# Kernel tuning notes

Hardware: AMD Instinct MI355X
Metric: run time of the kernel (lower is better)

The kernel has to match this reference:

```python
import jax, jax.numpy as jnp
import numpy as np

B, N, D, H = 1, 2048, 2048, 16
K = D // H  # head dim = 128


def setup_inputs() -> dict:
    key = jax.random.key(0)
    k1, k2, k3 = jax.random.split(key, 3)
    x = jax.random.normal(k1, (B, N, D), dtype=jnp.float32)
    # torch Linear(D, 3D, bias=False): y = x @ W.T; we store the transposed weight directly.
    W_qkv = jax.random.normal(k2, (D, 3 * D), dtype=jnp.float32) * 0.02
    W_out = jax.random.normal(k3, (D, D), dtype=jnp.float32) * 0.02
    return {"x": x, "W_qkv": W_qkv, "W_out": W_out}


def reference(x, W_qkv, W_out):
    b, n, d = x.shape
    qkv = (x @ W_qkv).reshape(b, n, 3, H, K)  # [B,N,3,H,K]
    q, k, v = qkv[:, :, 0], qkv[:, :, 1], qkv[:, :, 2]  # each [B,N,H,K]
    scale = np.float32(1.0 / np.sqrt(K))
    scores = jnp.einsum('bnhk,bmhk->bnhm', q, k) * scale  # [B,N,H,M]
    causal_mask = jnp.tril(jnp.ones((n, n), dtype=bool))  # [N,M]
    scores = jnp.where(causal_mask[None, :, None, :], scores, jnp.float32(-jnp.inf))
    probs = jax.nn.softmax(scores, axis=-1)
    attn = jnp.einsum('bnhm,bmhk->bnhk', probs, v).reshape(b, n, d)
    return attn @ W_out
```

## Files before the change

kernel.cpp:

```cpp
#include <hip/hip_runtime.h>
#include <hip/hip_bf16.h>
#include <math.h>

#define N_SEQ  2048
#define DMODEL 2048
#define NHEAD  16
#define HDIM   128
#define QKV_LD 6144

typedef __attribute__((ext_vector_type(8))) short bf16x8;
typedef __attribute__((ext_vector_type(4))) float f32x4;

__device__ __forceinline__ ushort f2bf(float x) {
    union { float f; unsigned u; } v; v.f = x;
    unsigned r = (v.u + 0x7fffu + ((v.u >> 16) & 1u)) >> 16;
    return (ushort)r;
}
__device__ __forceinline__ float bf2f(ushort h) {
    union { unsigned u; float f; } v; v.u = ((unsigned)h) << 16;
    return v.f;
}

__global__ __launch_bounds__(256)
void convert_split(const float* __restrict__ in, ushort* __restrict__ oh,
                   ushort* __restrict__ ol, int n4)
{
    int i = blockIdx.x * 256 + threadIdx.x;
    if (i >= n4) return;
    float4 v = ((const float4*)in)[i];
    ushort4 h, l;
    h.x = f2bf(v.x); l.x = f2bf(v.x - bf2f(h.x));
    h.y = f2bf(v.y); l.y = f2bf(v.y - bf2f(h.y));
    h.z = f2bf(v.z); l.z = f2bf(v.z - bf2f(h.z));
    h.w = f2bf(v.w); l.w = f2bf(v.w - bf2f(h.w));
    ((ushort4*)oh)[i] = h;
    ((ushort4*)ol)[i] = l;
}

__global__ __launch_bounds__(256)
void convert_split_t(const float* __restrict__ in, ushort* __restrict__ oh,
                     ushort* __restrict__ ol, int R, int C)
{
    __shared__ float T[64][65];
    const int t = threadIdx.x;
    const int c0 = blockIdx.x * 64, r0 = blockIdx.y * 64;
    #pragma unroll
    for (int p = 0; p < 4; ++p) {
        int r = (t >> 4) + p * 16;
        int c4 = (t & 15) * 4;
        float4 v = *(const float4*)&in[(size_t)(r0 + r) * C + c0 + c4];
        T[r][c4] = v.x; T[r][c4 + 1] = v.y; T[r][c4 + 2] = v.z; T[r][c4 + 3] = v.w;
    }
    __syncthreads();
    #pragma unroll
    for (int p = 0; p < 4; ++p) {
        int c = (t >> 4) + p * 16;
        int r4 = (t & 15) * 4;
        float f0 = T[r4][c], f1 = T[r4 + 1][c], f2 = T[r4 + 2][c], f3 = T[r4 + 3][c];
        ushort4 h, l;
        h.x = f2bf(f0); l.x = f2bf(f0 - bf2f(h.x));
        h.y = f2bf(f1); l.y = f2bf(f1 - bf2f(h.y));
        h.z = f2bf(f2); l.z = f2bf(f2 - bf2f(h.z));
        h.w = f2bf(f3); l.w = f2bf(f3 - bf2f(h.w));
        *(ushort4*)&oh[(size_t)(c0 + c) * R + r0 + r4] = h;
        *(ushort4*)&ol[(size_t)(c0 + c) * R + r0 + r4] = l;
    }
}

__global__ __launch_bounds__(256)
void transpose_v(const ushort* __restrict__ qkvh, ushort* __restrict__ vt)
{
    __shared__ ushort T[64][72];
    const int t = threadIdx.x;
    const int c0 = blockIdx.x * 64, n0 = blockIdx.y * 64;
    #pragma unroll
    for (int p = 0; p < 2; ++p) {
        int r = (t >> 3) + p * 32;
        int u = (t & 7) * 8;
        *(bf16x8*)&T[r][u] = *(const bf16x8*)&qkvh[(size_t)(n0 + r) * QKV_LD + 2 * DMODEL + c0 + u];
    }
    __syncthreads();
    #pragma unroll
    for (int p = 0; p < 2; ++p) {
        int d = (t >> 3) + p * 32;
        int ju = (t & 7) * 8;
        bf16x8 o;
        #pragma unroll
        for (int i = 0; i < 8; ++i) o[i] = (short)T[ju + i][d];
        *(bf16x8*)&vt[(size_t)(c0 + d) * N_SEQ + n0 + ju] = o;
    }
}

template<bool BF16OUT>
__global__ __launch_bounds__(256, 2)
void gemm_bf16x3(const ushort* __restrict__ Ah_g, const ushort* __restrict__ Al_g,
                 const ushort* __restrict__ Bh_g, const ushort* __restrict__ Bl_g,
                 ushort* __restrict__ Ch, ushort* __restrict__ Cl,
                 float* __restrict__ Cf, int M, int N, int K)
{
    __shared__ ushort Ah[128 * 40], Al[128 * 40], Bh[128 * 40], Bl[128 * 40];
    const int t = threadIdx.x;
    const int l = t & 63;
    const int w = t >> 6;
    const int l15 = l & 15, kgr = l >> 4;
    const int wm = (w >> 1) * 64, wn = (w & 1) * 64;
    const int bm = blockIdx.y * 128, bn = blockIdx.x * 128;
    const int sr = t >> 2, sku = (t & 3) * 8;

    f32x4 acc[4][4] = {};
    bf16x8 sA[4], sB[4];

    auto load_stage = [&](int k0) {
        const size_t a0 = (size_t)(bm + sr) * K + k0 + sku;
        const size_t a1 = (size_t)(bm + sr + 64) * K + k0 + sku;
        sA[0] = *(const bf16x8*)(Ah_g + a0);
        sA[1] = *(const bf16x8*)(Ah_g + a1);
        sA[2] = *(const bf16x8*)(Al_g + a0);
        sA[3] = *(const bf16x8*)(Al_g + a1);
        const size_t b0 = (size_t)(bn + sr) * K + k0 + sku;
        const size_t b1 = (size_t)(bn + sr + 64) * K + k0 + sku;
        sB[0] = *(const bf16x8*)(Bh_g + b0);
        sB[1] = *(const bf16x8*)(Bh_g + b1);
        sB[2] = *(const bf16x8*)(Bl_g + b0);
        sB[3] = *(const bf16x8*)(Bl_g + b1);
    };
    auto write_stage = [&]() {
        *(bf16x8*)&Ah[sr * 40 + sku]        = sA[0];
        *(bf16x8*)&Ah[(sr + 64) * 40 + sku] = sA[1];
        *(bf16x8*)&Al[sr * 40 + sku]        = sA[2];
        *(bf16x8*)&Al[(sr + 64) * 40 + sku] = sA[3];
        *(bf16x8*)&Bh[sr * 40 + sku]        = sB[0];
        *(bf16x8*)&Bh[(sr + 64) * 40 + sku] = sB[1];
        *(bf16x8*)&Bl[sr * 40 + sku]        = sB[2];
        *(bf16x8*)&Bl[(sr + 64) * 40 + sku] = sB[3];
    };

    load_stage(0);
    for (int k0 = 0; k0 < K; k0 += 32) {
        __syncthreads();
        write_stage();
        __syncthreads();
        if (k0 + 32 < K) load_stage(k0 + 32);

        bf16x8 ah[4], al[4], bh[4], bl[4];
        #pragma unroll
        for (int mf = 0; mf < 4; ++mf) {
            ah[mf] = *(const bf16x8*)&Ah[(wm + mf * 16 + l15) * 40 + kgr * 8];
            al[mf] = *(const bf16x8*)&Al[(wm + mf * 16 + l15) * 40 + kgr * 8];
        }
        #pragma unroll
        for (int nf = 0; nf < 4; ++nf) {
            bh[nf] = *(const bf16x8*)&Bh[(wn + nf * 16 + l15) * 40 + kgr * 8];
            bl[nf] = *(const bf16x8*)&Bl[(wn + nf * 16 + l15) * 40 + kgr * 8];
        }
        #pragma unroll
        for (int mf = 0; mf < 4; ++mf)
            #pragma unroll
            for (int nf = 0; nf < 4; ++nf) {
                acc[mf][nf] = __builtin_amdgcn_mfma_f32_16x16x32_bf16(ah[mf], bh[nf], acc[mf][nf], 0, 0, 0);
                acc[mf][nf] = __builtin_amdgcn_mfma_f32_16x16x32_bf16(ah[mf], bl[nf], acc[mf][nf], 0, 0, 0);
                acc[mf][nf] = __builtin_amdgcn_mfma_f32_16x16x32_bf16(al[mf], bh[nf], acc[mf][nf], 0, 0, 0);
            }
    }

    #pragma unroll
    for (int mf = 0; mf < 4; ++mf)
        #pragma unroll
        for (int nf = 0; nf < 4; ++nf)
            #pragma unroll
            for (int r = 0; r < 4; ++r) {
                const int m = bm + wm + mf * 16 + kgr * 4 + r;
                const int n = bn + wn + nf * 16 + l15;
                const float v = acc[mf][nf][r];
                if constexpr (BF16OUT) {
                    ushort h = f2bf(v);
                    Ch[(size_t)m * N + n] = h;
                    Cl[(size_t)m * N + n] = f2bf(v - bf2f(h));
                } else {
                    Cf[(size_t)m * N + n] = v;
                }
            }
}

__global__ __launch_bounds__(256, 2)
void attn_mfma(const ushort* __restrict__ qkvh, const ushort* __restrict__ qkvl,
               const ushort* __restrict__ vt,
               ushort* __restrict__ oh, ushort* __restrict__ ol)
{
    __shared__ ushort Kh[64 * 136], Kl[64 * 136], Vts[128 * 72], St[4 * 16 * 72];
    const int t = threadIdx.x;
    const int l = t & 63;
    const int w = t >> 6;
    const int l15 = l & 15, kgr = l >> 4;
    const int h = blockIdx.y, qb = blockIdx.x;
    const int q0 = qb * 64 + w * 16;

    bf16x8 qh[4], ql[4];
    {
        const size_t base = (size_t)(q0 + l15) * QKV_LD + h * HDIM;
        #pragma unroll
        for (int kc = 0; kc < 4; ++kc) {
            qh[kc] = *(const bf16x8*)(qkvh + base + kc * 32 + kgr * 8);
            ql[kc] = *(const bf16x8*)(qkvl + base + kc * 32 + kgr * 8);
        }
    }

    f32x4 o[8] = {};
    float m_run[4], l_run[4];
    #pragma unroll
    for (int r = 0; r < 4; ++r) { m_run[r] = -1e30f; l_run[r] = 0.f; }

    bf16x8 sKh[4], sKl[4], sV[4];
    auto load_tile = [&](int jb) {
        #pragma unroll
        for (int i = 0; i < 4; ++i) {
            int r = (t >> 4) + i * 16;
            size_t g = (size_t)(jb + r) * QKV_LD + DMODEL + h * HDIM + (t & 15) * 8;
            sKh[i] = *(const bf16x8*)(qkvh + g);
            sKl[i] = *(const bf16x8*)(qkvl + g);
        }
        #pragma unroll
        for (int i = 0; i < 4; ++i) {
            int d = (t >> 3) + i * 32;
            sV[i] = *(const bf16x8*)(vt + (size_t)(h * HDIM + d) * N_SEQ + jb + (t & 7) * 8);
        }
    };
    auto write_tile = [&]() {
        #pragma unroll
        for (int i = 0; i < 4; ++i) {
            int r = (t >> 4) + i * 16;
            *(bf16x8*)&Kh[r * 136 + (t & 15) * 8] = sKh[i];
            *(bf16x8*)&Kl[r * 136 + (t & 15) * 8] = sKl[i];
        }
        #pragma unroll
        for (int i = 0; i < 4; ++i) {
            int d = (t >> 3) + i * 32;
            *(bf16x8*)&Vts[d * 72 + (t & 7) * 8] = sV[i];
        }
    };

    const float scale = 0.08838834764831845f;

    load_tile(0);
    for (int jt = 0; jt <= qb; ++jt) {
        const int jb = jt * 64;
        __syncthreads();
        write_tile();
        __syncthreads();
        if (jt < qb) load_tile(jb + 64);

        float sv[4][4];
        #pragma unroll
        for (int jf = 0; jf < 4; ++jf) {
            f32x4 sacc = {};
            #pragma unroll
            for (int kc = 0; kc < 4; ++kc) {
                bf16x8 kh = *(const bf16x8*)&Kh[(jf * 16 + l15) * 136 + kc * 32 + kgr * 8];
                bf16x8 kl = *(const bf16x8*)&Kl[(jf * 16 + l15) * 136 + kc * 32 + kgr * 8];
                sacc = __builtin_amdgcn_mfma_f32_16x16x32_bf16(qh[kc], kh, sacc, 0, 0, 0);
                sacc = __builtin_amdgcn_mfma_f32_16x16x32_bf16(qh[kc], kl, sacc, 0, 0, 0);
                sacc = __builtin_amdgcn_mfma_f32_16x16x32_bf16(ql[kc], kh, sacc, 0, 0, 0);
            }
            const int j = jb + jf * 16 + l15;
            #pragma unroll
            for (int r = 0; r < 4; ++r) {
                const int q = q0 + kgr * 4 + r;
                sv[jf][r] = (j > q) ? -1e30f : sacc[r] * scale;
            }
        }

        float corr[4], p[4][4];
        #pragma unroll
        for (int r = 0; r < 4; ++r) {
            float tm = fmaxf(fmaxf(sv[0][r], sv[1][r]), fmaxf(sv[2][r], sv[3][r]));
            tm = fmaxf(tm, __shfl_xor(tm, 1));
            tm = fmaxf(tm, __shfl_xor(tm, 2));
            tm = fmaxf(tm, __shfl_xor(tm, 4));
            tm = fmaxf(tm, __shfl_xor(tm, 8));
            const float nm = fmaxf(m_run[r], tm);
            corr[r] = __expf(m_run[r] - nm);
            m_run[r] = nm;
            float rs = 0.f;
            #pragma unroll
            for (int jf = 0; jf < 4; ++jf) { p[jf][r] = __expf(sv[jf][r] - nm); rs += p[jf][r]; }
            rs += __shfl_xor(rs, 1);
            rs += __shfl_xor(rs, 2);
            rs += __shfl_xor(rs, 4);
            rs += __shfl_xor(rs, 8);
            l_run[r] = l_run[r] * corr[r] + rs;
        }

        #pragma unroll
        for (int jf = 0; jf < 4; ++jf)
            #pragma unroll
            for (int r = 0; r < 4; ++r)
                St[w * 1152 + (kgr * 4 + r) * 72 + jf * 16 + l15] = f2bf(p[jf][r]);

        #pragma unroll
        for (int df = 0; df < 8; ++df)
            #pragma unroll
            for (int r = 0; r < 4; ++r) o[df][r] *= corr[r];

        #pragma unroll
        for (int jc = 0; jc < 2; ++jc) {
            bf16x8 pa = *(const bf16x8*)&St[w * 1152 + l15 * 72 + jc * 32 + kgr * 8];
            #pragma unroll
            for (int df = 0; df < 8; ++df) {
                bf16x8 vb = *(const bf16x8*)&Vts[(df * 16 + l15) * 72 + jc * 32 + kgr * 8];
                o[df] = __builtin_amdgcn_mfma_f32_16x16x32_bf16(pa, vb, o[df], 0, 0, 0);
            }
        }
    }

    #pragma unroll
    for (int r = 0; r < 4; ++r) l_run[r] = 1.f / l_run[r];
    #pragma unroll
    for (int df = 0; df < 8; ++df)
        #pragma unroll
        for (int r = 0; r < 4; ++r) {
            const float v = o[df][r] * l_run[r];
            const size_t a = (size_t)(q0 + kgr * 4 + r) * DMODEL + h * HDIM + df * 16 + l15;
            const ushort hh = f2bf(v);
            oh[a] = hh;
            ol[a] = f2bf(v - bf2f(hh));
        }
}

#define BM 128
#define BN 128
#define BKG 16

__global__ __launch_bounds__(256, 2)
void gemm_f32(const float* __restrict__ A, const float* __restrict__ B,
              float* __restrict__ C, int M, int N, int K,
              int lda, int ldb, int ldc)
{
    __shared__ float As[BKG][132];
    __shared__ float Bs[BKG][132];
    const int t = threadIdx.x;
    const int tx = t & 15, ty = t >> 4;
    const int bm = blockIdx.y * BM, bn = blockIdx.x * BN;
    const int am = t >> 2, ak = (t & 3) << 2;
    const int bk = t >> 5, bn4 = (t & 31) << 2;
    float acc[8][8];
    #pragma unroll
    for (int i = 0; i < 8; ++i)
        #pragma unroll
        for (int j = 0; j < 8; ++j) acc[i][j] = 0.f;
    for (int k0 = 0; k0 < K; k0 += BKG) {
        const float4 a0 = *(const float4*)&A[(size_t)(bm + am) * lda + k0 + ak];
        const float4 a1 = *(const float4*)&A[(size_t)(bm + am + 64) * lda + k0 + ak];
        const float4 b0 = *(const float4*)&B[(size_t)(k0 + bk) * ldb + bn + bn4];
        const float4 b1 = *(const float4*)&B[(size_t)(k0 + bk + 8) * ldb + bn + bn4];
        __syncthreads();
        As[ak + 0][am] = a0.x; As[ak + 1][am] = a0.y; As[ak + 2][am] = a0.z; As[ak + 3][am] = a0.w;
        As[ak + 0][am + 64] = a1.x; As[ak + 1][am + 64] = a1.y; As[ak + 2][am + 64] = a1.z; As[ak + 3][am + 64] = a1.w;
        *(float4*)&Bs[bk][bn4] = b0;
        *(float4*)&Bs[bk + 8][bn4] = b1;
        __syncthreads();
        #pragma unroll
        for (int kk = 0; kk < BKG; ++kk) {
            const float4 A0 = *(const float4*)&As[kk][ty << 2];
            const float4 A1 = *(const float4*)&As[kk][(ty << 2) + 64];
            const float4 B0 = *(const float4*)&Bs[kk][tx << 2];
            const float4 B1 = *(const float4*)&Bs[kk][(tx << 2) + 64];
            const float a[8] = {A0.x, A0.y, A0.z, A0.w, A1.x, A1.y, A1.z, A1.w};
            const float b[8] = {B0.x, B0.y, B0.z, B0.w, B1.x, B1.y, B1.z, B1.w};
            #pragma unroll
            for (int i = 0; i < 8; ++i)
                #pragma unroll
                for (int j = 0; j < 8; ++j) acc[i][j] = fmaf(a[i], b[j], acc[i][j]);
        }
    }
    #pragma unroll
    for (int i = 0; i < 8; ++i) {
        const int m = bm + ((i < 4) ? ((ty << 2) + i) : (64 + (ty << 2) + i - 4));
        const float4 o0 = make_float4(acc[i][0], acc[i][1], acc[i][2], acc[i][3]);
        const float4 o1 = make_float4(acc[i][4], acc[i][5], acc[i][6], acc[i][7]);
        *(float4*)&C[(size_t)m * ldc + bn + (tx << 2)] = o0;
        *(float4*)&C[(size_t)m * ldc + bn + 64 + (tx << 2)] = o1;
    }
}

#define QB 64
#define KB 64
#define PQT 68

__device__ __forceinline__ int swz(int c, int k) { return c ^ ((k >> 3) & 7); }

__global__ __launch_bounds__(256, 1)
void attn_f32(const float* __restrict__ qkv, float* __restrict__ out)
{
    __shared__ float Qt[HDIM][PQT];
    __shared__ float Kt[HDIM][PQT];
    __shared__ float Vs[KB][132];
    __shared__ float Sf[KB][PQT];
    __shared__ float pmax[4][QB];
    __shared__ float psum[4][QB];
    __shared__ float rowm[QB];
    __shared__ float rowstat[QB];
    const int t = threadIdx.x;
    const int h = blockIdx.y, qb = blockIdx.x;
    const int row0 = qb * QB;
    const int lc = t & 31, lr = t >> 5;
    {
        const float* qbase = qkv + (size_t)row0 * QKV_LD + h * HDIM;
        #pragma unroll
        for (int r = 0; r < 8; ++r) {
            const int m = lr + r * 8;
            const float4 q = *(const float4*)&qbase[(size_t)m * QKV_LD + (lc << 2)];
            const int kb4 = lc << 2;
            Qt[kb4 + 0][(swz(m >> 2, kb4 + 0) << 2) + (m & 3)] = q.x;
            Qt[kb4 + 1][(swz(m >> 2, kb4 + 1) << 2) + (m & 3)] = q.y;
            Qt[kb4 + 2][(swz(m >> 2, kb4 + 2) << 2) + (m & 3)] = q.z;
            Qt[kb4 + 3][(swz(m >> 2, kb4 + 3) << 2) + (m & 3)] = q.w;
        }
    }
    float m_run = -3.0e38f, l_run = 0.f;
    float o[4][8];
    #pragma unroll
    for (int i = 0; i < 4; ++i)
        #pragma unroll
        for (int j = 0; j < 8; ++j) o[i][j] = 0.f;
    const int cq = t & 15, cj = t >> 4;
    const int om = (t >> 4) << 2, oc = (t & 15) << 2;
    const int srow = t & 63, sseg = t >> 6;
    const float scale = 0.08838834764831845f;
    const int ntiles = qb + 1;
    for (int jt = 0; jt < ntiles; ++jt) {
        const int jbase = jt * KB;
        float4 kreg[8], vreg[8];
        {
            const float* kbaseg = qkv + (size_t)jbase * QKV_LD + DMODEL + h * HDIM;
            const float* vbaseg = qkv + (size_t)jbase * QKV_LD + 2 * DMODEL + h * HDIM;
            #pragma unroll
            for (int r = 0; r < 8; ++r) {
                const int j = lr + r * 8;
                kreg[r] = *(const float4*)&kbaseg[(size_t)j * QKV_LD + (lc << 2)];
                vreg[r] = *(const float4*)&vbaseg[(size_t)j * QKV_LD + (lc << 2)];
            }
        }
        __syncthreads();
        {
            const int kb4 = lc << 2;
            #pragma unroll
            for (int r = 0; r < 8; ++r) {
                const int j = lr + r * 8;
                Kt[kb4 + 0][(swz(j >> 2, kb4 + 0) << 2) + (j & 3)] = kreg[r].x;
                Kt[kb4 + 1][(swz(j >> 2, kb4 + 1) << 2) + (j & 3)] = kreg[r].y;
                Kt[kb4 + 2][(swz(j >> 2, kb4 + 2) << 2) + (j & 3)] = kreg[r].z;
                Kt[kb4 + 3][(swz(j >> 2, kb4 + 3) << 2) + (j & 3)] = kreg[r].w;
                *(float4*)&Vs[j][kb4] = vreg[r];
            }
        }
        __syncthreads();
        float s[4][4];
        #pragma unroll
        for (int i = 0; i < 4; ++i)
            #pragma unroll
            for (int j = 0; j < 4; ++j) s[i][j] = 0.f;
        #pragma unroll 8
        for (int k = 0; k < HDIM; ++k) {
            const float4 qv = *(const float4*)&Qt[k][swz(cq, k) << 2];
            const float4 kv = *(const float4*)&Kt[k][swz(cj, k) << 2];
            const float qa[4] = {qv.x, qv.y, qv.z, qv.w};
            const float ka[4] = {kv.x, kv.y, kv.z, kv.w};
            #pragma unroll
            for (int mm = 0; mm < 4; ++mm)
                #pragma unroll
                for (int jj = 0; jj < 4; ++jj) s[mm][jj] = fmaf(qa[mm], ka[jj], s[mm][jj]);
        }
        const bool diag = (jt == qb);
        #pragma unroll
        for (int jj = 0; jj < 4; ++jj)
            #pragma unroll
            for (int mm = 0; mm < 4; ++mm) {
                float v = s[mm][jj] * scale;
                if (diag && (jbase + (cj << 2) + jj > row0 + (cq << 2) + mm)) v = -1.0e30f;
                Sf[(cj << 2) + jj][(cq << 2) + mm] = v;
            }
        __syncthreads();
        {
            float tmax = -3.0e38f;
            #pragma unroll
            for (int i = 0; i < 16; ++i) tmax = fmaxf(tmax, Sf[(sseg << 4) + i][srow]);
            pmax[sseg][srow] = tmax;
        }
        __syncthreads();
        if (t < QB) {
            float nm = fmaxf(fmaxf(pmax[0][t], pmax[1][t]), fmaxf(pmax[2][t], pmax[3][t]));
            nm = fmaxf(m_run, nm);
            rowm[t] = nm;
            rowstat[t] = __expf(m_run - nm);
            m_run = nm;
        }
        __syncthreads();
        {
            const float nm = rowm[srow];
            float rsum = 0.f;
            #pragma unroll
            for (int i = 0; i < 16; ++i) {
                const int j = (sseg << 4) + i;
                const float p = __expf(Sf[j][srow] - nm);
                Sf[j][srow] = p;
                rsum += p;
            }
            psum[sseg][srow] = rsum;
        }
        __syncthreads();
        if (t < QB) {
            l_run = l_run * rowstat[t] + (psum[0][t] + psum[1][t] + psum[2][t] + psum[3][t]);
        }
        {
            const float c0 = rowstat[om + 0], c1 = rowstat[om + 1];
            const float c2 = rowstat[om + 2], c3 = rowstat[om + 3];
            #pragma unroll
            for (int c = 0; c < 8; ++c) { o[0][c] *= c0; o[1][c] *= c1; o[2][c] *= c2; o[3][c] *= c3; }
            #pragma unroll 4
            for (int j = 0; j < KB; ++j) {
                const float4 p = *(const float4*)&Sf[j][om];
                const float4 v0 = *(const float4*)&Vs[j][oc];
                const float4 v1 = *(const float4*)&Vs[j][oc + 64];
                const float pa[4] = {p.x, p.y, p.z, p.w};
                const float va[8] = {v0.x, v0.y, v0.z, v0.w, v1.x, v1.y, v1.z, v1.w};
                #pragma unroll
                for (int mm = 0; mm < 4; ++mm)
                    #pragma unroll
                    for (int c = 0; c < 8; ++c) o[mm][c] = fmaf(pa[mm], va[c], o[mm][c]);
            }
        }
    }
    __syncthreads();
    if (t < QB) rowstat[t] = 1.f / l_run;
    __syncthreads();
    float* obase = out + (size_t)row0 * DMODEL + h * HDIM;
    #pragma unroll
    for (int mm = 0; mm < 4; ++mm) {
        const float inv = rowstat[om + mm];
        const float4 r0 = make_float4(o[mm][0] * inv, o[mm][1] * inv, o[mm][2] * inv, o[mm][3] * inv);
        const float4 r1 = make_float4(o[mm][4] * inv, o[mm][5] * inv, o[mm][6] * inv, o[mm][7] * inv);
        *(float4*)&obase[(size_t)(om + mm) * DMODEL + oc] = r0;
        *(float4*)&obase[(size_t)(om + mm) * DMODEL + 64 + oc] = r1;
    }
}

extern "C" void kernel_launch(void* const* d_in, const int* in_sizes, int n_in,
                              void* d_out, int out_size, void* d_ws, size_t ws_size,
                              hipStream_t stream)
{
    const float* x    = (const float*)d_in[0];
    const float* Wqkv = (const float*)d_in[1];
    const float* Wout = (const float*)d_in[2];
    float* outp = (float*)d_out;

    const size_t O_XHI = 0;
    const size_t O_XLO = 8388608;
    const size_t O_WT  = 16777216;
    const size_t O_QKV = 67108864;
    const size_t NEED  = 117440512;

    char* ws = (char*)d_ws;
    if (ws_size >= NEED) {
        ushort* x_hi   = (ushort*)(ws + O_XHI);
        ushort* x_lo   = (ushort*)(ws + O_XLO);
        ushort* wqt_hi = (ushort*)(ws + O_WT);
        ushort* wqt_lo = (ushort*)(ws + O_WT + 25165824);
        ushort* qkv_hi = (ushort*)(ws + O_QKV);
        ushort* qkv_lo = (ushort*)(ws + O_QKV + 25165824);
        ushort* wot_hi = (ushort*)(ws + O_WT);
        ushort* wot_lo = (ushort*)(ws + O_WT + 8388608);
        ushort* vt     = (ushort*)(ws + O_WT + 16777216);
        ushort* at_hi  = (ushort*)(ws + O_XHI);
        ushort* at_lo  = (ushort*)(ws + O_XLO);

        convert_split<<<dim3(N_SEQ * DMODEL / 4 / 256), 256, 0, stream>>>(
            x, x_hi, x_lo, N_SEQ * DMODEL / 4);
        convert_split_t<<<dim3(QKV_LD / 64, DMODEL / 64), 256, 0, stream>>>(
            Wqkv, wqt_hi, wqt_lo, DMODEL, QKV_LD);
        gemm_bf16x3<true><<<dim3(QKV_LD / 128, N_SEQ / 128), 256, 0, stream>>>(
            x_hi, x_lo, wqt_hi, wqt_lo, qkv_hi, qkv_lo, nullptr,
            N_SEQ, QKV_LD, DMODEL);
        convert_split_t<<<dim3(DMODEL / 64, DMODEL / 64), 256, 0, stream>>>(
            Wout, wot_hi, wot_lo, DMODEL, DMODEL);
        transpose_v<<<dim3(DMODEL / 64, N_SEQ / 64), 256, 0, stream>>>(qkv_hi, vt);
        attn_mfma<<<dim3(N_SEQ / 64, NHEAD), 256, 0, stream>>>(
            qkv_hi, qkv_lo, vt, at_hi, at_lo);
        gemm_bf16x3<false><<<dim3(DMODEL / 128, N_SEQ / 128), 256, 0, stream>>>(
            at_hi, at_lo, wot_hi, wot_lo, nullptr, nullptr, outp,
            N_SEQ, DMODEL, DMODEL);
    } else {
        float* qkv  = (float*)d_ws;
        float* attn = qkv + (size_t)N_SEQ * QKV_LD;
        gemm_f32<<<dim3(QKV_LD / BN, N_SEQ / BM), 256, 0, stream>>>(
            x, Wqkv, qkv, N_SEQ, QKV_LD, DMODEL, DMODEL, QKV_LD, QKV_LD);
        attn_f32<<<dim3(N_SEQ / QB, NHEAD), 256, 0, stream>>>(qkv, attn);
        gemm_f32<<<dim3(DMODEL / BN, N_SEQ / BM), 256, 0, stream>>>(
            attn, Wout, outp, N_SEQ, DMODEL, DMODEL, DMODEL, DMODEL, DMODEL);
    }
}
```

Before: 474.2 us.

## Add 256x256-tile double-buffered bf16x3 GEMM for QKV projection

Replaces the QKV projection GEMM with a new kernel using 256x256 tiles, 512 threads, double-buffered LDS with register prefetch, and an XCD-grouped block index remap. Hi/lo split data are interleaved per row in LDS. The goal is more data reuse per tile and loads that overlap compute. The trade-off is a large LDS footprint and only 192 workgroups, fewer than the CU count. The fp32 fallback path is also removed.

```diff
diff --git a/kernel.cpp b/kernel.cpp
--- a/kernel.cpp
+++ b/kernel.cpp
@@ -89,6 +89,109 @@
         for (int i = 0; i < 8; ++i) o[i] = (short)T[ju + i][d];
         *(bf16x8*)&vt[(size_t)(c0 + d) * N_SEQ + n0 + ju] = o;
     }
+}
+
+#define GBM 256
+#define GBN 256
+#define GBK 32
+#define GPITCH 68
+
+template<bool BF16OUT>
+__global__ __launch_bounds__(512, 2)
+void gemm_bf16x3_v2(const ushort* __restrict__ Ah_g, const ushort* __restrict__ Al_g,
+                    const ushort* __restrict__ Bh_g, const ushort* __restrict__ Bl_g,
+                    ushort* __restrict__ Ch, ushort* __restrict__ Cl,
+                    float* __restrict__ Cf, int M, int N, int K)
+{
+    __shared__ ushort bufA[2][GBM * GPITCH];
+    __shared__ ushort bufB[2][GBN * GPITCH];
+
+    const int t = threadIdx.x;
+    const int l = t & 63;
+    const int w = t >> 6;
+    const int l15 = l & 15, kgr = l >> 4;
+    const int wm = (w >> 2) * 128;
+    const int wn = (w & 3) * 64;
+
+    const int nbx = N / GBN, nby = M / GBM;
+    const int nwg = nbx * nby;
+    int flat = blockIdx.x + blockIdx.y * nbx;
+    if ((nwg & 7) == 0) flat = (flat & 7) * (nwg >> 3) + (flat >> 3);
+    const int bm = (flat / nbx) * GBM;
+    const int bn = (flat % nbx) * GBN;
+
+    const int rA = t >> 1;
+    const int hA = t & 1;
+    const ushort* gA = (hA ? Al_g : Ah_g) + (size_t)(bm + rA) * K;
+    const ushort* gB = (hA ? Bl_g : Bh_g) + (size_t)(bn + rA) * K;
+
+    bf16x8 stA[4], stB[4];
+    auto load_regs = [&](int k0) {
+        #pragma unroll
+        for (int j = 0; j < 4; ++j) {
+            stA[j] = *(const bf16x8*)(gA + k0 + j * 8);
+            stB[j] = *(const bf16x8*)(gB + k0 + j * 8);
+        }
+    };
+    auto write_lds = [&](int b) {
+        #pragma unroll
+        for (int j = 0; j < 4; ++j) {
+            *(bf16x8*)&bufA[b][rA * GPITCH + hA * 32 + j * 8] = stA[j];
+            *(bf16x8*)&bufB[b][rA * GPITCH + hA * 32 + j * 8] = stB[j];
+        }
+    };
+
+    f32x4 acc[8][4] = {};
+
+    const int nt = K / GBK;
+    load_regs(0);
+    write_lds(0);
+    load_regs(GBK);
+
+    for (int i = 0; i < nt; ++i) {
+        const int c = i & 1;
+        asm volatile("s_waitcnt lgkmcnt(0)\n\ts_barrier" ::: "memory");
+        if (i + 1 < nt) write_lds(c ^ 1);
+        if (i + 2 < nt) load_regs((i + 2) * GBK);
+
+        bf16x8 bh[4], bl[4];
+        #pragma unroll
+        for (int nf = 0; nf < 4; ++nf) {
+            const int r = wn + nf * 16 + l15;
+            bh[nf] = *(const bf16x8*)&bufB[c][r * GPITCH + kgr * 8];
+            bl[nf] = *(const bf16x8*)&bufB[c][r * GPITCH + 32 + kgr * 8];
+        }
+        #pragma unroll
+        for (int mf = 0; mf < 8; ++mf) {
+            const int r = wm + mf * 16 + l15;
+            bf16x8 ah = *(const bf16x8*)&bufA[c][r * GPITCH + kgr * 8];
+            bf16x8 al = *(const bf16x8*)&bufA[c][r * GPITCH + 32 + kgr * 8];
+            #pragma unroll
+            for (int nf = 0; nf < 4; ++nf) {
+                acc[mf][nf] = __builtin_amdgcn_mfma_f32_16x16x32_bf16(ah, bh[nf], acc[mf][nf], 0, 0, 0);
+                acc[mf][nf] = __builtin_amdgcn_mfma_f32_16x16x32_bf16(ah, bl[nf], acc[mf][nf], 0, 0, 0);
+                acc[mf][nf] = __builtin_amdgcn_mfma_f32_16x16x32_bf16(al, bh[nf], acc[mf][nf], 0, 0, 0);
+            }
+        }
+    }
+
+    #pragma unroll
+    for (int mf = 0; mf < 8; ++mf)
+        #pragma unroll
+        for (int nf = 0; nf < 4; ++nf)
+            #pragma unroll
+            for (int r = 0; r < 4; ++r) {
+                const int m = bm + wm + mf * 16 + kgr * 4 + r;
+                const int n = bn + wn + nf * 16 + l15;
+                const float v = acc[mf][nf][r];
+                if constexpr (BF16OUT) {
+                    ushort h = f2bf(v);
+                    Ch[(size_t)m * N + n] = h;
+                    Cl[(size_t)m * N + n] = f2bf(v - bf2f(h));
+                } else {
+                    Cf[(size_t)m * N + n] = v;
+                }
+            }
 }
 
 template<bool BF16OUT>
@@ -326,224 +429,6 @@
         }
 }
 
-#define BM 128
-#define BN 128
-#define BKG 16
-
-__global__ __launch_bounds__(256, 2)
-void gemm_f32(const float* __restrict__ A, const float* __restrict__ B,
-              float* __restrict__ C, int M, int N, int K,
-              int lda, int ldb, int ldc)
-{
-    __shared__ float As[BKG][132];
-    __shared__ float Bs[BKG][132];
-    const int t = threadIdx.x;
-    const int tx = t & 15, ty = t >> 4;
-    const int bm = blockIdx.y * BM, bn = blockIdx.x * BN;
-    const int am = t >> 2, ak = (t & 3) << 2;
-    const int bk = t >> 5, bn4 = (t & 31) << 2;
-    float acc[8][8];
-    #pragma unroll
-    for (int i = 0; i < 8; ++i)
-        #pragma unroll
-        for (int j = 0; j < 8; ++j) acc[i][j] = 0.f;
-    for (int k0 = 0; k0 < K; k0 += BKG) {
-        const float4 a0 = *(const float4*)&A[(size_t)(bm + am) * lda + k0 + ak];
-        const float4 a1 = *(const float4*)&A[(size_t)(bm + am + 64) * lda + k0 + ak];
-        const float4 b0 = *(const float4*)&B[(size_t)(k0 + bk) * ldb + bn + bn4];
-        const float4 b1 = *(const float4*)&B[(size_t)(k0 + bk + 8) * ldb + bn + bn4];
-        __syncthreads();
-        As[ak + 0][am] = a0.x; As[ak + 1][am] = a0.y; As[ak + 2][am] = a0.z; As[ak + 3][am] = a0.w;
-        As[ak + 0][am + 64] = a1.x; As[ak + 1][am + 64] = a1.y; As[ak + 2][am + 64] = a1.z; As[ak + 3][am + 64] = a1.w;
-        *(float4*)&Bs[bk][bn4] = b0;
-        *(float4*)&Bs[bk + 8][bn4] = b1;
-        __syncthreads();
-        #pragma unroll
-        for (int kk = 0; kk < BKG; ++kk) {
-            const float4 A0 = *(const float4*)&As[kk][ty << 2];
-            const float4 A1 = *(const float4*)&As[kk][(ty << 2) + 64];
-            const float4 B0 = *(const float4*)&Bs[kk][tx << 2];
-            const float4 B1 = *(const float4*)&Bs[kk][(tx << 2) + 64];
-            const float a[8] = {A0.x, A0.y, A0.z, A0.w, A1.x, A1.y, A1.z, A1.w};
-            const float b[8] = {B0.x, B0.y, B0.z, B0.w, B1.x, B1.y, B1.z, B1.w};
-            #pragma unroll
-            for (int i = 0; i < 8; ++i)
-                #pragma unroll
-                for (int j = 0; j < 8; ++j) acc[i][j] = fmaf(a[i], b[j], acc[i][j]);
-        }
-    }
-    #pragma unroll
-    for (int i = 0; i < 8; ++i) {
-        const int m = bm + ((i < 4) ? ((ty << 2) + i) : (64 + (ty << 2) + i - 4));
-        const float4 o0 = make_float4(acc[i][0], acc[i][1], acc[i][2], acc[i][3]);
-        const float4 o1 = make_float4(acc[i][4], acc[i][5], acc[i][6], acc[i][7]);
-        *(float4*)&C[(size_t)m * ldc + bn + (tx << 2)] = o0;
-        *(float4*)&C[(size_t)m * ldc + bn + 64 + (tx << 2)] = o1;
-    }
-}
-
-#define QB 64
-#define KB 64
-#define PQT 68
-
-__device__ __forceinline__ int swz(int c, int k) { return c ^ ((k >> 3) & 7); }
-
-__global__ __launch_bounds__(256, 1)
-void attn_f32(const float* __restrict__ qkv, float* __restrict__ out)
-{
-    __shared__ float Qt[HDIM][PQT];
-    __shared__ float Kt[HDIM][PQT];
-    __shared__ float Vs[KB][132];
-    __shared__ float Sf[KB][PQT];
-    __shared__ float pmax[4][QB];
-    __shared__ float psum[4][QB];
-    __shared__ float rowm[QB];
-    __shared__ float rowstat[QB];
-    const int t = threadIdx.x;
-    const int h = blockIdx.y, qb = blockIdx.x;
-    const int row0 = qb * QB;
-    const int lc = t & 31, lr = t >> 5;
-    {
-        const float* qbase = qkv + (size_t)row0 * QKV_LD + h * HDIM;
-        #pragma unroll
-        for (int r = 0; r < 8; ++r) {
-            const int m = lr + r * 8;
-            const float4 q = *(const float4*)&qbase[(size_t)m * QKV_LD + (lc << 2)];
-            const int kb4 = lc << 2;
-            Qt[kb4 + 0][(swz(m >> 2, kb4 + 0) << 2) + (m & 3)] = q.x;
-            Qt[kb4 + 1][(swz(m >> 2, kb4 + 1) << 2) + (m & 3)] = q.y;
-            Qt[kb4 + 2][(swz(m >> 2, kb4 + 2) << 2) + (m & 3)] = q.z;
-            Qt[kb4 + 3][(swz(m >> 2, kb4 + 3) << 2) + (m & 3)] = q.w;
-        }
-    }
-    float m_run = -3.0e38f, l_run = 0.f;
-    float o[4][8];
-    #pragma unroll
-    for (int i = 0; i < 4; ++i)
-        #pragma unroll
-        for (int j = 0; j < 8; ++j) o[i][j] = 0.f;
-    const int cq = t & 15, cj = t >> 4;
-    const int om = (t >> 4) << 2, oc = (t & 15) << 2;
-    const int srow = t & 63, sseg = t >> 6;
-    const float scale = 0.08838834764831845f;
-    const int ntiles = qb + 1;
-    for (int jt = 0; jt < ntiles; ++jt) {
-        const int jbase = jt * KB;
-        float4 kreg[8], vreg[8];
-        {
-            const float* kbaseg = qkv + (size_t)jbase * QKV_LD + DMODEL + h * HDIM;
-            const float* vbaseg = qkv + (size_t)jbase * QKV_LD + 2 * DMODEL + h * HDIM;
-            #pragma unroll
-            for (int r = 0; r < 8; ++r) {
-                const int j = lr + r * 8;
-                kreg[r] = *(const float4*)&kbaseg[(size_t)j * QKV_LD + (lc << 2)];
-                vreg[r] = *(const float4*)&vbaseg[(size_t)j * QKV_LD + (lc << 2)];
-            }
-        }
-        __syncthreads();
-        {
-            const int kb4 = lc << 2;
-            #pragma unroll
-            for (int r = 0; r < 8; ++r) {
-                const int j = lr + r * 8;
-                Kt[kb4 + 0][(swz(j >> 2, kb4 + 0) << 2) + (j & 3)] = kreg[r].x;
-                Kt[kb4 + 1][(swz(j >> 2, kb4 + 1) << 2) + (j & 3)] = kreg[r].y;
-                Kt[kb4 + 2][(swz(j >> 2, kb4 + 2) << 2) + (j & 3)] = kreg[r].z;
-                Kt[kb4 + 3][(swz(j >> 2, kb4 + 3) << 2) + (j & 3)] = kreg[r].w;
-                *(float4*)&Vs[j][kb4] = vreg[r];
-            }
-        }
-        __syncthreads();
-        float s[4][4];
-        #pragma unroll
-        for (int i = 0; i < 4; ++i)
-            #pragma unroll
-            for (int j = 0; j < 4; ++j) s[i][j] = 0.f;
-        #pragma unroll 8
-        for (int k = 0; k < HDIM; ++k) {
-            const float4 qv = *(const float4*)&Qt[k][swz(cq, k) << 2];
-            const float4 kv = *(const float4*)&Kt[k][swz(cj, k) << 2];
-            const float qa[4] = {qv.x, qv.y, qv.z, qv.w};
-            const float ka[4] = {kv.x, kv.y, kv.z, kv.w};
-            #pragma unroll
-            for (int mm = 0; mm < 4; ++mm)
-                #pragma unroll
-                for (int jj = 0; jj < 4; ++jj) s[mm][jj] = fmaf(qa[mm], ka[jj], s[mm][jj]);
-        }
-        const bool diag = (jt == qb);
-        #pragma unroll
-        for (int jj = 0; jj < 4; ++jj)
-            #pragma unroll
-            for (int mm = 0; mm < 4; ++mm) {
-                float v = s[mm][jj] * scale;
-                if (diag && (jbase + (cj << 2) + jj > row0 + (cq << 2) + mm)) v = -1.0e30f;
-                Sf[(cj << 2) + jj][(cq << 2) + mm] = v;
-            }
-        __syncthreads();
-        {
-            float tmax = -3.0e38f;
-            #pragma unroll
-            for (int i = 0; i < 16; ++i) tmax = fmaxf(tmax, Sf[(sseg << 4) + i][srow]);
-            pmax[sseg][srow] = tmax;
-        }
-        __syncthreads();
-        if (t < QB) {
-            float nm = fmaxf(fmaxf(pmax[0][t], pmax[1][t]), fmaxf(pmax[2][t], pmax[3][t]));
-            nm = fmaxf(m_run, nm);
-            rowm[t] = nm;
-            rowstat[t] = __expf(m_run - nm);
-            m_run = nm;
-        }
-        __syncthreads();
-        {
-            const float nm = rowm[srow];
-            float rsum = 0.f;
-            #pragma unroll
-            for (int i = 0; i < 16; ++i) {
-                const int j = (sseg << 4) + i;
-                const float p = __expf(Sf[j][srow] - nm);
-                Sf[j][srow] = p;
-                rsum += p;
-            }
-            psum[sseg][srow] = rsum;
-        }
-        __syncthreads();
-        if (t < QB) {
-            l_run = l_run * rowstat[t] + (psum[0][t] + psum[1][t] + psum[2][t] + psum[3][t]);
-        }
-        {
-            const float c0 = rowstat[om + 0], c1 = rowstat[om + 1];
-            const float c2 = rowstat[om + 2], c3 = rowstat[om + 3];
-            #pragma unroll
-            for (int c = 0; c < 8; ++c) { o[0][c] *= c0; o[1][c] *= c1; o[2][c] *= c2; o[3][c] *= c3; }
-            #pragma unroll 4
-            for (int j = 0; j < KB; ++j) {
-                const float4 p = *(const float4*)&Sf[j][om];
-                const float4 v0 = *(const float4*)&Vs[j][oc];
-                const float4 v1 = *(const float4*)&Vs[j][oc + 64];
-                const float pa[4] = {p.x, p.y, p.z, p.w};
-                const float va[8] = {v0.x, v0.y, v0.z, v0.w, v1.x, v1.y, v1.z, v1.w};
-                #pragma unroll
-                for (int mm = 0; mm < 4; ++mm)
-                    #pragma unroll
-                    for (int c = 0; c < 8; ++c) o[mm][c] = fmaf(pa[mm], va[c], o[mm][c]);
-            }
-        }
-    }
-    __syncthreads();
-    if (t < QB) rowstat[t] = 1.f / l_run;
-    __syncthreads();
-    float* obase = out + (size_t)row0 * DMODEL + h * HDIM;
-    #pragma unroll
-    for (int mm = 0; mm < 4; ++mm) {
-        const float inv = rowstat[om + mm];
-        const float4 r0 = make_float4(o[mm][0] * inv, o[mm][1] * inv, o[mm][2] * inv, o[mm][3] * inv);
-        const float4 r1 = make_float4(o[mm][4] * inv, o[mm][5] * inv, o[mm][6] * inv, o[mm][7] * inv);
-        *(float4*)&obase[(size_t)(om + mm) * DMODEL + oc] = r0;
-        *(float4*)&obase[(size_t)(om + mm) * DMODEL + 64 + oc] = r1;
-    }
-}
-
 extern "C" void kernel_launch(void* const* d_in, const int* in_sizes, int n_in,
                               void* d_out, int out_size, void* d_ws, size_t ws_size,
                               hipStream_t stream)
@@ -557,44 +442,33 @@
     const size_t O_XLO = 8388608;
     const size_t O_WT  = 16777216;
     const size_t O_QKV = 67108864;
-    const size_t NEED  = 117440512;
 
     char* ws = (char*)d_ws;
-    if (ws_size >= NEED) {
-        ushort* x_hi   = (ushort*)(ws + O_XHI);
-        ushort* x_lo   = (ushort*)(ws + O_XLO);
-        ushort* wqt_hi = (ushort*)(ws + O_WT);
-        ushort* wqt_lo = (ushort*)(ws + O_WT + 25165824);
-        ushort* qkv_hi = (ushort*)(ws + O_QKV);
-        ushort* qkv_lo = (ushort*)(ws + O_QKV + 25165824);
-        ushort* wot_hi = (ushort*)(ws + O_WT);
-        ushort* wot_lo = (ushort*)(ws + O_WT + 8388608);
-        ushort* vt     = (ushort*)(ws + O_WT + 16777216);
-        ushort* at_hi  = (ushort*)(ws + O_XHI);
-        ushort* at_lo  = (ushort*)(ws + O_XLO);
-
-        convert_split<<<dim3(N_SEQ * DMODEL / 4 / 256), 256, 0, stream>>>(
-            x, x_hi, x_lo, N_SEQ * DMODEL / 4);
-        convert_split_t<<<dim3(QKV_LD / 64, DMODEL / 64), 256, 0, stream>>>(
-            Wqkv, wqt_hi, wqt_lo, DMODEL, QKV_LD);
-        gemm_bf16x3<true><<<dim3(QKV_LD / 128, N_SEQ / 128), 256, 0, stream>>>(
-            x_hi, x_lo, wqt_hi, wqt_lo, qkv_hi, qkv_lo, nullptr,
-            N_SEQ, QKV_LD, DMODEL);
-        convert_split_t<<<dim3(DMODEL / 64, DMODEL / 64), 256, 0, stream>>>(
-            Wout, wot_hi, wot_lo, DMODEL, DMODEL);
-        transpose_v<<<dim3(DMODEL / 64, N_SEQ / 64), 256, 0, stream>>>(qkv_hi, vt);
-        attn_mfma<<<dim3(N_SEQ / 64, NHEAD), 256, 0, stream>>>(
-            qkv_hi, qkv_lo, vt, at_hi, at_lo);
-        gemm_bf16x3<false><<<dim3(DMODEL / 128, N_SEQ / 128), 256, 0, stream>>>(
-            at_hi, at_lo, wot_hi, wot_lo, nullptr, nullptr, outp,
-            N_SEQ, DMODEL, DMODEL);
-    } else {
-        float* qkv  = (float*)d_ws;
-        float* attn = qkv + (size_t)N_SEQ * QKV_LD;
-        gemm_f32<<<dim3(QKV_LD / BN, N_SEQ / BM), 256, 0, stream>>>(
-            x, Wqkv, qkv, N_SEQ, QKV_LD, DMODEL, DMODEL, QKV_LD, QKV_LD);
-        attn_f32<<<dim3(N_SEQ / QB, NHEAD), 256, 0, stream>>>(qkv, attn);
-        gemm_f32<<<dim3(DMODEL / BN, N_SEQ / BM), 256, 0, stream>>>(
-            attn, Wout, outp, N_SEQ, DMODEL, DMODEL, DMODEL, DMODEL, DMODEL);
-    }
-}
+    ushort* x_hi   = (ushort*)(ws + O_XHI);
+    ushort* x_lo   = (ushort*)(ws + O_XLO);
+    ushort* wqt_hi = (ushort*)(ws + O_WT);
+    ushort* wqt_lo = (ushort*)(ws + O_WT + 25165824);
+    ushort* qkv_hi = (ushort*)(ws + O_QKV);
+    ushort* qkv_lo = (ushort*)(ws + O_QKV + 25165824);
+    ushort* wot_hi = (ushort*)(ws + O_WT);
+    ushort* wot_lo = (ushort*)(ws + O_WT + 8388608);
+    ushort* vt     = (ushort*)(ws + O_WT + 16777216);
+    ushort* at_hi  = (ushort*)(ws + O_XHI);
+    ushort* at_lo  = (ushort*)(ws + O_XLO);
+
+    convert_split<<<dim3(N_SEQ * DMODEL / 4 / 256), 256, 0, stream>>>(
+        x, x_hi, x_lo, N_SEQ * DMODEL / 4);
+    convert_split_t<<<dim3(QKV_LD / 64, DMODEL / 64), 256, 0, stream>>>(
+        Wqkv, wqt_hi, wqt_lo, DMODEL, QKV_LD);
+    gemm_bf16x3_v2<true><<<dim3(QKV_LD / GBN, N_SEQ / GBM), 512, 0, stream>>>(
+        x_hi, x_lo, wqt_hi, wqt_lo, qkv_hi, qkv_lo, nullptr,
+        N_SEQ, QKV_LD, DMODEL);
+    convert_split_t<<<dim3(DMODEL / 64, DMODEL / 64), 256, 0, stream>>>(
+        Wout, wot_hi, wot_lo, DMODEL, DMODEL);
+    transpose_v<<<dim3(DMODEL / 64, N_SEQ / 64), 256, 0, stream>>>(qkv_hi, vt);
+    attn_mfma<<<dim3(N_SEQ / 64, NHEAD), 256, 0, stream>>>(
+        qkv_hi, qkv_lo, vt, at_hi, at_lo);
+    gemm_bf16x3<false><<<dim3(DMODEL / 128, N_SEQ / 128), 256, 0, stream>>>(
+        at_hi, at_lo, wot_hi, wot_lo, nullptr, nullptr, outp,
+        N_SEQ, DMODEL, DMODEL);
+}
```

Result: slower. 519.3 us (+9.5%).
